# Kernel tuning notes

Measured on AMD Instinct MI355X. Metric: run time of the kernel, lower is better.

## Reference

```python
import jax, jax.numpy as jnp
import numpy as np

TEMPERATURE = 1.0
EPS = 1e-5
COS_EPS = 1e-8  # torch CosineSimilarity default eps
N_POS, N_NEG, D = 512, 512, 512


def setup_inputs() -> dict:
    key = jax.random.key(0)
    k1, k2, k3 = jax.random.split(key, 3)
    tensor_positive = jax.random.normal(k1, (N_POS, D), dtype=jnp.float32)
    tensor_negative = jax.random.normal(k2, (N_NEG, D), dtype=jnp.float32)
    # nn.Linear(512*3, 1), weight ~ N(0, 0.02^2), bias zeros
    linear_w = jax.random.normal(k3, (1, 3 * D), dtype=jnp.float32) * 0.02
    linear_b = jnp.zeros((1,), dtype=jnp.float32)
    return {"tensor_positive": tensor_positive, "tensor_negative": tensor_negative,
            "linear_w": linear_w, "linear_b": linear_b}


def _cos_matrix(a, b):
    # pairwise cosine similarity [Na, Nb], matching torch CosineSimilarity eps clamp
    an = a / jnp.maximum(jnp.linalg.norm(a, axis=-1, keepdims=True), COS_EPS)
    bn = b / jnp.maximum(jnp.linalg.norm(b, axis=-1, keepdims=True), COS_EPS)
    return an @ bn.T


def reference(tensor_positive, tensor_negative, linear_w, linear_b):
    pos, neg = tensor_positive, tensor_negative
    n_pos, d = pos.shape
    n_neg = neg.shape[0]

    # NCE part
    logit_n = jnp.exp(_cos_matrix(pos, neg) / TEMPERATURE)        # [N, M]
    deno_n = jnp.sum(logit_n, axis=-1)                            # [N]
    logit_p = jnp.exp(_cos_matrix(pos, pos) / TEMPERATURE)        # [N, N]
    loss = jnp.sum(-jnp.log(logit_p / (deno_n[:, None] + logit_p + EPS)))

    # Pairwise classifier: linear(cat([a, b, |a-b|])) decomposed as
    # a@w1 + b@w2 + |a-b|@w3 to avoid materializing the 3D concat.
    w = linear_w[0]
    w1, w2, w3 = w[:d], w[d:2 * d], w[2 * d:]
    allv = jnp.concatenate([pos, neg], axis=0)                    # [N+M, D]
    t1 = pos @ w1                                                 # [N]
    t2 = allv @ w2                                                # [N+M]
    diff = jnp.abs(pos[:, None, :] - allv[None, :, :])            # [N, N+M, D]
    t3 = jnp.einsum('nmd,d->nm', diff, w3)                        # [N, N+M]
    logits = t1[:, None] + t2[None, :] + t3 + linear_b[0]
    labels = jnp.concatenate([jnp.ones((n_pos,), jnp.float32),
                              jnp.zeros((n_neg,), jnp.float32)])  # [N+M]
    # BCE(sigmoid(logits), labels), stable form; per-i mean then sum over i
    bce = labels[None, :] * jax.nn.softplus(-logits) + (1.0 - labels[None, :]) * jax.nn.softplus(logits)
    loss = loss + jnp.sum(jnp.mean(bce, axis=1))
    return loss
```

## Files before the change

kernel.cpp:

```cpp
#include <hip/hip_runtime.h>
#include <math.h>

#define NPOS 512
#define DIM  512
#define NB   1024
#define EPSV 1e-5f
#define COS_EPS 1e-8f

#define OFF_INV 0
#define OFF_T1  1024
#define OFF_T2  1536
#define OFF_P   2560
#define PSZ     (NPOS * NB)

__device__ __forceinline__ float softplus_f(float x) {
    return fmaxf(x, 0.f) + __logf(1.f + __expf(-fabsf(x)));
}

__global__ __launch_bounds__(256) void prep_kernel(
    const float* __restrict__ pos, const float* __restrict__ neg,
    const float* __restrict__ w, float* __restrict__ ws, float* __restrict__ out)
{
    int gtid = blockIdx.x * 256 + threadIdx.x;
    if (gtid == 0) out[0] = 0.f;
    int row  = gtid >> 6;
    int lane = threadIdx.x & 63;
    if (row >= NB) return;
    bool is_pos = row < NPOS;
    const float* r = is_pos ? pos + row * DIM : neg + (row - NPOS) * DIM;

    const float4* r4  = (const float4*)r + lane * 2;
    const float4* w14 = (const float4*)(w) + lane * 2;
    const float4* w24 = (const float4*)(w + DIM) + lane * 2;
    float4 a0 = r4[0],  a1 = r4[1];
    float4 u0 = w14[0], u1 = w14[1];
    float4 v0 = w24[0], v1 = w24[1];

    float ss  = a0.x*a0.x + a0.y*a0.y + a0.z*a0.z + a0.w*a0.w
              + a1.x*a1.x + a1.y*a1.y + a1.z*a1.z + a1.w*a1.w;
    float dw1 = a0.x*u0.x + a0.y*u0.y + a0.z*u0.z + a0.w*u0.w
              + a1.x*u1.x + a1.y*u1.y + a1.z*u1.z + a1.w*u1.w;
    float dw2 = a0.x*v0.x + a0.y*v0.y + a0.z*v0.z + a0.w*v0.w
              + a1.x*v1.x + a1.y*v1.y + a1.z*v1.z + a1.w*v1.w;

    #pragma unroll
    for (int off = 32; off; off >>= 1) {
        ss  += __shfl_xor(ss, off);
        dw1 += __shfl_xor(dw1, off);
        dw2 += __shfl_xor(dw2, off);
    }
    if (lane == 0) {
        float inv = 1.f / fmaxf(sqrtf(ss), COS_EPS);
        ws[OFF_INV + row] = inv;
        ws[OFF_T2 + row]  = dw2;
        if (is_pos) ws[OFF_T1 + row] = dw1;
    }
}

__global__ __launch_bounds__(256) void fused_kernel(
    const float* __restrict__ pos, const float* __restrict__ neg,
    const float* __restrict__ w, float* __restrict__ ws)
{
    __shared__ __align__(16) float As[64][36];
    __shared__ __align__(16) float Bs[64][36];

    const int tid = threadIdx.x;
    const int n0 = blockIdx.y * 64;
    const int m0 = blockIdx.x * 64;
    const int z  = blockIdx.z;
    const float* Asrc = pos + (size_t)n0 * DIM + z * 128;
    const float* Bsrc = ((m0 < NPOS) ? (pos + (size_t)m0 * DIM)
                                     : (neg + (size_t)(m0 - NPOS) * DIM)) + z * 128;
    const float* w3 = w + 2 * DIM + z * 128;

    const int lr = tid >> 3;
    const int lc = (tid & 7) << 2;
    const int ti = tid >> 4;
    const int tj = tid & 15;

    float c[4][4] = {{0.f}}, t[4][4] = {{0.f}};

    float4 a0 = *(const float4*)(Asrc + lr * DIM + lc);
    float4 a1 = *(const float4*)(Asrc + (lr + 32) * DIM + lc);
    float4 b0 = *(const float4*)(Bsrc + lr * DIM + lc);
    float4 b1 = *(const float4*)(Bsrc + (lr + 32) * DIM + lc);
    *(float4*)&As[lr][lc]      = a0;
    *(float4*)&As[lr + 32][lc] = a1;
    *(float4*)&Bs[lr][lc]      = b0;
    *(float4*)&Bs[lr + 32][lc] = b1;
    __syncthreads();

    #pragma unroll 1
    for (int iter = 0; iter < 4; ++iter) {
        const bool more = (iter < 3);
        if (more) {
            const float* ap = Asrc + (iter + 1) * 32;
            const float* bp = Bsrc + (iter + 1) * 32;
            a0 = *(const float4*)(ap + lr * DIM + lc);
            a1 = *(const float4*)(ap + (lr + 32) * DIM + lc);
            b0 = *(const float4*)(bp + lr * DIM + lc);
            b1 = *(const float4*)(bp + (lr + 32) * DIM + lc);
        }
        const float* w3i = w3 + iter * 32;
        #pragma unroll
        for (int k = 0; k < 32; k += 4) {
            float4 av[4], bv[4];
            #pragma unroll
            for (int r = 0; r < 4; ++r) av[r] = *(const float4*)&As[ti + 16 * r][k];
            #pragma unroll
            for (int s = 0; s < 4; ++s) bv[s] = *(const float4*)&Bs[tj + 16 * s][k];
            const float4 wv = *(const float4*)(w3i + k);
            #pragma unroll
            for (int r = 0; r < 4; ++r) {
                #pragma unroll
                for (int s = 0; s < 4; ++s) {
                    c[r][s] = fmaf(av[r].x, bv[s].x, c[r][s]);
                    c[r][s] = fmaf(av[r].y, bv[s].y, c[r][s]);
                    c[r][s] = fmaf(av[r].z, bv[s].z, c[r][s]);
                    c[r][s] = fmaf(av[r].w, bv[s].w, c[r][s]);
                    t[r][s] = fmaf(fabsf(av[r].x - bv[s].x), wv.x, t[r][s]);
                    t[r][s] = fmaf(fabsf(av[r].y - bv[s].y), wv.y, t[r][s]);
                    t[r][s] = fmaf(fabsf(av[r].z - bv[s].z), wv.z, t[r][s]);
                    t[r][s] = fmaf(fabsf(av[r].w - bv[s].w), wv.w, t[r][s]);
                }
            }
        }
        if (more) {
            __syncthreads();
            *(float4*)&As[lr][lc]      = a0;
            *(float4*)&As[lr + 32][lc] = a1;
            *(float4*)&Bs[lr][lc]      = b0;
            *(float4*)&Bs[lr + 32][lc] = b1;
            __syncthreads();
        }
    }

    float* Sp = ws + OFF_P + (size_t)z * PSZ;
    float* Tp = ws + OFF_P + (size_t)(4 + z) * PSZ;
    #pragma unroll
    for (int r = 0; r < 4; ++r) {
        int n = n0 + ti + 16 * r;
        #pragma unroll
        for (int s = 0; s < 4; ++s) {
            int m = m0 + tj + 16 * s;
            Sp[(size_t)n * NB + m] = c[r][s];
            Tp[(size_t)n * NB + m] = t[r][s];
        }
    }
}

__global__ __launch_bounds__(256) void finish_kernel(
    const float* __restrict__ lb, float* __restrict__ ws, float* __restrict__ out)
{
    const int n = blockIdx.x * 4 + (threadIdx.x >> 6);
    const int l = threadIdx.x & 63;
    const float invn = ws[OFF_INV + n];
    const float t1n  = ws[OFF_T1 + n];
    const float bias = lb[0];

    float4 cj[4];
    float eneg = 0.f;
    #pragma unroll
    for (int j = 0; j < 4; ++j) {
        int i4 = l + 64 * j;
        float4 sc = {0.f, 0.f, 0.f, 0.f};
        #pragma unroll
        for (int z = 0; z < 4; ++z) {
            const float4 s = ((const float4*)(ws + OFF_P + (size_t)z * PSZ + (size_t)n * NB))[i4];
            sc.x += s.x; sc.y += s.y; sc.z += s.z; sc.w += s.w;
        }
        float4 inv4 = *(const float4*)(ws + OFF_INV + 4 * i4);
        float4 cc;
        cc.x = sc.x * invn * inv4.x;
        cc.y = sc.y * invn * inv4.y;
        cc.z = sc.z * invn * inv4.z;
        cc.w = sc.w * invn * inv4.w;
        cj[j] = cc;
        if (j >= 2)
            eneg += __expf(cc.x) + __expf(cc.y) + __expf(cc.z) + __expf(cc.w);
    }
    #pragma unroll
    for (int off = 32; off; off >>= 1) eneg += __shfl_xor(eneg, off);

    float part = 0.f;
    #pragma unroll
    for (int j = 0; j < 2; ++j) {
        float4 cc = cj[j];
        part += __logf(eneg + __expf(cc.x) + EPSV) - cc.x;
        part += __logf(eneg + __expf(cc.y) + EPSV) - cc.y;
        part += __logf(eneg + __expf(cc.z) + EPSV) - cc.z;
        part += __logf(eneg + __expf(cc.w) + EPSV) - cc.w;
    }

    float bce = 0.f;
    #pragma unroll
    for (int j = 0; j < 4; ++j) {
        int i4 = l + 64 * j;
        float4 tt = {0.f, 0.f, 0.f, 0.f};
        #pragma unroll
        for (int z = 0; z < 4; ++z) {
            const float4 p = ((const float4*)(ws + OFF_P + (size_t)(4 + z) * PSZ + (size_t)n * NB))[i4];
            tt.x += p.x; tt.y += p.y; tt.z += p.z; tt.w += p.w;
        }
        float4 t2 = *(const float4*)(ws + OFF_T2 + 4 * i4);
        float4 lg;
        lg.x = t1n + t2.x + tt.x + bias;
        lg.y = t1n + t2.y + tt.y + bias;
        lg.z = t1n + t2.z + tt.z + bias;
        lg.w = t1n + t2.w + tt.w + bias;
        if (j < 2)
            bce += softplus_f(-lg.x) + softplus_f(-lg.y) + softplus_f(-lg.z) + softplus_f(-lg.w);
        else
            bce += softplus_f(lg.x) + softplus_f(lg.y) + softplus_f(lg.z) + softplus_f(lg.w);
    }
    part += bce * (1.f / 1024.f);

    #pragma unroll
    for (int off = 32; off; off >>= 1) part += __shfl_xor(part, off);
    if (l == 0) atomicAdd(out, part);
}

extern "C" void kernel_launch(void* const* d_in, const int* in_sizes, int n_in,
                              void* d_out, int out_size, void* d_ws, size_t ws_size,
                              hipStream_t stream) {
    (void)in_sizes; (void)n_in; (void)out_size; (void)ws_size;
    const float* pos = (const float*)d_in[0];
    const float* neg = (const float*)d_in[1];
    const float* w   = (const float*)d_in[2];
    const float* lb  = (const float*)d_in[3];
    float* out = (float*)d_out;
    float* ws  = (float*)d_ws;

    prep_kernel<<<256, 256, 0, stream>>>(pos, neg, w, ws, out);
    fused_kernel<<<dim3(16, 8, 4), 256, 0, stream>>>(pos, neg, w, ws);
    finish_kernel<<<128, 256, 0, stream>>>(lb, ws, out);
}
```

Baseline: 109.4 us.

## Use 128x128 register tiles with 8-way K split and one-row finish blocks

Enlarges the fused kernel tile to 128x128 outputs per block with 8x8 accumulators per thread, and splits K into 8 slices of 64 loaded into shared memory once. This raises FMA-to-LDS-load ratio and removes the in-loop reload and syncs. In exchange it doubles the partial-sum workspace written and reread, cuts the grid to 256 blocks, and raises register pressure. The finish kernel is reorganized so each block handles one row with a shared-memory reduction.

```diff
diff --git a/kernel.cpp b/kernel.cpp
--- a/kernel.cpp
+++ b/kernel.cpp
@@ -57,91 +57,69 @@
     }
 }
 
-__global__ __launch_bounds__(256) void fused_kernel(
+__global__ __launch_bounds__(256, 1) void fused_kernel(
     const float* __restrict__ pos, const float* __restrict__ neg,
     const float* __restrict__ w, float* __restrict__ ws)
 {
-    __shared__ __align__(16) float As[64][36];
-    __shared__ __align__(16) float Bs[64][36];
+    __shared__ __align__(16) float As[128][68];
+    __shared__ __align__(16) float Bs[128][68];
 
     const int tid = threadIdx.x;
-    const int n0 = blockIdx.y * 64;
-    const int m0 = blockIdx.x * 64;
+    const int m0 = blockIdx.x * 128;
+    const int n0 = blockIdx.y * 128;
     const int z  = blockIdx.z;
-    const float* Asrc = pos + (size_t)n0 * DIM + z * 128;
+
+    const float* Asrc = pos + (size_t)n0 * DIM + z * 64;
     const float* Bsrc = ((m0 < NPOS) ? (pos + (size_t)m0 * DIM)
-                                     : (neg + (size_t)(m0 - NPOS) * DIM)) + z * 128;
-    const float* w3 = w + 2 * DIM + z * 128;
-
-    const int lr = tid >> 3;
-    const int lc = (tid & 7) << 2;
+                                     : (neg + (size_t)(m0 - NPOS) * DIM)) + z * 64;
+    const float* w3 = w + 2 * DIM + z * 64;
+
+    const int lr = tid >> 4;
+    const int lc = (tid & 15) << 2;
+    #pragma unroll
+    for (int q = 0; q < 8; ++q) {
+        int row = lr + 16 * q;
+        *(float4*)&As[row][lc] = *(const float4*)(Asrc + (size_t)row * DIM + lc);
+        *(float4*)&Bs[row][lc] = *(const float4*)(Bsrc + (size_t)row * DIM + lc);
+    }
+    __syncthreads();
+
     const int ti = tid >> 4;
     const int tj = tid & 15;
 
-    float c[4][4] = {{0.f}}, t[4][4] = {{0.f}};
-
-    float4 a0 = *(const float4*)(Asrc + lr * DIM + lc);
-    float4 a1 = *(const float4*)(Asrc + (lr + 32) * DIM + lc);
-    float4 b0 = *(const float4*)(Bsrc + lr * DIM + lc);
-    float4 b1 = *(const float4*)(Bsrc + (lr + 32) * DIM + lc);
-    *(float4*)&As[lr][lc]      = a0;
-    *(float4*)&As[lr + 32][lc] = a1;
-    *(float4*)&Bs[lr][lc]      = b0;
-    *(float4*)&Bs[lr + 32][lc] = b1;
-    __syncthreads();
-
-    #pragma unroll 1
-    for (int iter = 0; iter < 4; ++iter) {
-        const bool more = (iter < 3);
-        if (more) {
-            const float* ap = Asrc + (iter + 1) * 32;
-            const float* bp = Bsrc + (iter + 1) * 32;
-            a0 = *(const float4*)(ap + lr * DIM + lc);
-            a1 = *(const float4*)(ap + (lr + 32) * DIM + lc);
-            b0 = *(const float4*)(bp + lr * DIM + lc);
-            b1 = *(const float4*)(bp + (lr + 32) * DIM + lc);
-        }
-        const float* w3i = w3 + iter * 32;
+    float c[8][8] = {{0.f}};
+    float t[8][8] = {{0.f}};
+
+    #pragma unroll 2
+    for (int k = 0; k < 64; k += 4) {
+        const float4 wv = *(const float4*)(w3 + k);
+        float4 bv[8];
         #pragma unroll
-        for (int k = 0; k < 32; k += 4) {
-            float4 av[4], bv[4];
+        for (int s = 0; s < 8; ++s) bv[s] = *(const float4*)&Bs[tj + 16 * s][k];
+        #pragma unroll
+        for (int r = 0; r < 8; ++r) {
+            const float4 av = *(const float4*)&As[ti + 16 * r][k];
             #pragma unroll
-            for (int r = 0; r < 4; ++r) av[r] = *(const float4*)&As[ti + 16 * r][k];
-            #pragma unroll
-            for (int s = 0; s < 4; ++s) bv[s] = *(const float4*)&Bs[tj + 16 * s][k];
-            const float4 wv = *(const float4*)(w3i + k);
-            #pragma unroll
-            for (int r = 0; r < 4; ++r) {
-                #pragma unroll
-                for (int s = 0; s < 4; ++s) {
-                    c[r][s] = fmaf(av[r].x, bv[s].x, c[r][s]);
-                    c[r][s] = fmaf(av[r].y, bv[s].y, c[r][s]);
-                    c[r][s] = fmaf(av[r].z, bv[s].z, c[r][s]);
-                    c[r][s] = fmaf(av[r].w, bv[s].w, c[r][s]);
-                    t[r][s] = fmaf(fabsf(av[r].x - bv[s].x), wv.x, t[r][s]);
-                    t[r][s] = fmaf(fabsf(av[r].y - bv[s].y), wv.y, t[r][s]);
-                    t[r][s] = fmaf(fabsf(av[r].z - bv[s].z), wv.z, t[r][s]);
-                    t[r][s] = fmaf(fabsf(av[r].w - bv[s].w), wv.w, t[r][s]);
-                }
+            for (int s = 0; s < 8; ++s) {
+                c[r][s] = fmaf(av.x, bv[s].x, c[r][s]);
+                c[r][s] = fmaf(av.y, bv[s].y, c[r][s]);
+                c[r][s] = fmaf(av.z, bv[s].z, c[r][s]);
+                c[r][s] = fmaf(av.w, bv[s].w, c[r][s]);
+                t[r][s] = fmaf(fabsf(av.x - bv[s].x), wv.x, t[r][s]);
+                t[r][s] = fmaf(fabsf(av.y - bv[s].y), wv.y, t[r][s]);
+                t[r][s] = fmaf(fabsf(av.z - bv[s].z), wv.z, t[r][s]);
+                t[r][s] = fmaf(fabsf(av.w - bv[s].w), wv.w, t[r][s]);
             }
         }
-        if (more) {
-            __syncthreads();
-            *(float4*)&As[lr][lc]      = a0;
-            *(float4*)&As[lr + 32][lc] = a1;
-            *(float4*)&Bs[lr][lc]      = b0;
-            *(float4*)&Bs[lr + 32][lc] = b1;
-            __syncthreads();
-        }
     }
 
     float* Sp = ws + OFF_P + (size_t)z * PSZ;
-    float* Tp = ws + OFF_P + (size_t)(4 + z) * PSZ;
-    #pragma unroll
-    for (int r = 0; r < 4; ++r) {
+    float* Tp = ws + OFF_P + (size_t)(8 + z) * PSZ;
+    #pragma unroll
+    for (int r = 0; r < 8; ++r) {
         int n = n0 + ti + 16 * r;
         #pragma unroll
-        for (int s = 0; s < 4; ++s) {
+        for (int s = 0; s < 8; ++s) {
             int m = m0 + tj + 16 * s;
             Sp[(size_t)n * NB + m] = c[r][s];
             Tp[(size_t)n * NB + m] = t[r][s];
@@ -150,74 +128,71 @@
 }
 
 __global__ __launch_bounds__(256) void finish_kernel(
-    const float* __restrict__ lb, float* __restrict__ ws, float* __restrict__ out)
+    const float* __restrict__ lb, const float* __restrict__ ws, float* __restrict__ out)
 {
-    const int n = blockIdx.x * 4 + (threadIdx.x >> 6);
-    const int l = threadIdx.x & 63;
+    __shared__ float eneg_s[4];
+    __shared__ float red[4];
+
+    const int n  = blockIdx.x;
+    const int wv = threadIdx.x >> 6;
+    const int l  = threadIdx.x & 63;
+    const int i4 = wv * 64 + l;
+
+    float4 sc = {0.f, 0.f, 0.f, 0.f};
+    float4 tt = {0.f, 0.f, 0.f, 0.f};
+    #pragma unroll
+    for (int z = 0; z < 8; ++z) {
+        const float4 s = ((const float4*)(ws + OFF_P + (size_t)z * PSZ + (size_t)n * NB))[i4];
+        const float4 p = ((const float4*)(ws + OFF_P + (size_t)(8 + z) * PSZ + (size_t)n * NB))[i4];
+        sc.x += s.x; sc.y += s.y; sc.z += s.z; sc.w += s.w;
+        tt.x += p.x; tt.y += p.y; tt.z += p.z; tt.w += p.w;
+    }
+
     const float invn = ws[OFF_INV + n];
-    const float t1n  = ws[OFF_T1 + n];
-    const float bias = lb[0];
-
-    float4 cj[4];
-    float eneg = 0.f;
-    #pragma unroll
-    for (int j = 0; j < 4; ++j) {
-        int i4 = l + 64 * j;
-        float4 sc = {0.f, 0.f, 0.f, 0.f};
-        #pragma unroll
-        for (int z = 0; z < 4; ++z) {
-            const float4 s = ((const float4*)(ws + OFF_P + (size_t)z * PSZ + (size_t)n * NB))[i4];
-            sc.x += s.x; sc.y += s.y; sc.z += s.z; sc.w += s.w;
-        }
-        float4 inv4 = *(const float4*)(ws + OFF_INV + 4 * i4);
-        float4 cc;
-        cc.x = sc.x * invn * inv4.x;
-        cc.y = sc.y * invn * inv4.y;
-        cc.z = sc.z * invn * inv4.z;
-        cc.w = sc.w * invn * inv4.w;
-        cj[j] = cc;
-        if (j >= 2)
-            eneg += __expf(cc.x) + __expf(cc.y) + __expf(cc.z) + __expf(cc.w);
-    }
-    #pragma unroll
-    for (int off = 32; off; off >>= 1) eneg += __shfl_xor(eneg, off);
+    const float4 inv4 = *(const float4*)(ws + OFF_INV + 4 * i4);
+    float4 cc;
+    cc.x = sc.x * invn * inv4.x;
+    cc.y = sc.y * invn * inv4.y;
+    cc.z = sc.z * invn * inv4.z;
+    cc.w = sc.w * invn * inv4.w;
+
+    float ep = 0.f;
+    if (wv >= 2)
+        ep = __expf(cc.x) + __expf(cc.y) + __expf(cc.z) + __expf(cc.w);
+    #pragma unroll
+    for (int off = 32; off; off >>= 1) ep += __shfl_xor(ep, off);
+    if (l == 0) eneg_s[wv] = ep;
+    __syncthreads();
+    const float eneg = eneg_s[2] + eneg_s[3];
 
     float part = 0.f;
-    #pragma unroll
-    for (int j = 0; j < 2; ++j) {
-        float4 cc = cj[j];
+    if (wv < 2) {
         part += __logf(eneg + __expf(cc.x) + EPSV) - cc.x;
         part += __logf(eneg + __expf(cc.y) + EPSV) - cc.y;
         part += __logf(eneg + __expf(cc.z) + EPSV) - cc.z;
         part += __logf(eneg + __expf(cc.w) + EPSV) - cc.w;
     }
 
-    float bce = 0.f;
-    #pragma unroll
-    for (int j = 0; j < 4; ++j) {
-        int i4 = l + 64 * j;
-        float4 tt = {0.f, 0.f, 0.f, 0.f};
-        #pragma unroll
-        for (int z = 0; z < 4; ++z) {
-            const float4 p = ((const float4*)(ws + OFF_P + (size_t)(4 + z) * PSZ + (size_t)n * NB))[i4];
-            tt.x += p.x; tt.y += p.y; tt.z += p.z; tt.w += p.w;
-        }
-        float4 t2 = *(const float4*)(ws + OFF_T2 + 4 * i4);
-        float4 lg;
-        lg.x = t1n + t2.x + tt.x + bias;
-        lg.y = t1n + t2.y + tt.y + bias;
-        lg.z = t1n + t2.z + tt.z + bias;
-        lg.w = t1n + t2.w + tt.w + bias;
-        if (j < 2)
-            bce += softplus_f(-lg.x) + softplus_f(-lg.y) + softplus_f(-lg.z) + softplus_f(-lg.w);
-        else
-            bce += softplus_f(lg.x) + softplus_f(lg.y) + softplus_f(lg.z) + softplus_f(lg.w);
-    }
-    part += bce * (1.f / 1024.f);
+    const float t1n  = ws[OFF_T1 + n];
+    const float bias = lb[0];
+    const float4 t2 = *(const float4*)(ws + OFF_T2 + 4 * i4);
+    float lgx = t1n + t2.x + tt.x + bias;
+    float lgy = t1n + t2.y + tt.y + bias;
+    float lgz = t1n + t2.z + tt.z + bias;
+    float lgw = t1n + t2.w + tt.w + bias;
+    float b;
+    if (wv < 2)
+        b = softplus_f(-lgx) + softplus_f(-lgy) + softplus_f(-lgz) + softplus_f(-lgw);
+    else
+        b = softplus_f(lgx) + softplus_f(lgy) + softplus_f(lgz) + softplus_f(lgw);
+    part += b * (1.f / 1024.f);
 
     #pragma unroll
     for (int off = 32; off; off >>= 1) part += __shfl_xor(part, off);
-    if (l == 0) atomicAdd(out, part);
+    if (l == 0) red[wv] = part;
+    __syncthreads();
+    if (threadIdx.x == 0)
+        atomicAdd(out, red[0] + red[1] + red[2] + red[3]);
 }
 
 extern "C" void kernel_launch(void* const* d_in, const int* in_sizes, int n_in,
@@ -232,6 +207,6 @@
     float* ws  = (float*)d_ws;
 
     prep_kernel<<<256, 256, 0, stream>>>(pos, neg, w, ws, out);
-    fused_kernel<<<dim3(16, 8, 4), 256, 0, stream>>>(pos, neg, w, ws);
-    finish_kernel<<<128, 256, 0, stream>>>(lb, ws, out);
-}
+    fused_kernel<<<dim3(8, 4, 8), 256, 0, stream>>>(pos, neg, w, ws);
+    finish_kernel<<<512, 256, 0, stream>>>(lb, ws, out);
+}
```

Result: slower. 120.9 us (+10.5%).
